# Optimization experiments

Measured on AMD Instinct MI355X. Metric: run time of the kernel, lower is better.

Reference implementation:

```python
import jax, jax.numpy as jnp
import numpy as np

B, N, E_PER_G = 32, 2048, 16384
NF, NHID, NCLS = 128, 128, 10
RATIO = 0.5
NT = B * N
E = B * E_PER_G
K1 = int(np.ceil(RATIO * N))        # 1024 nodes kept per graph after pool1
K2 = int(np.ceil(RATIO * K1))       # 512
K3 = int(np.ceil(RATIO * K2))       # 256


def setup_inputs() -> dict:
    key = jax.random.key(0)
    ks = jax.random.split(key, 16)
    x = jax.random.normal(ks[0], (NT, NF), dtype=jnp.float32)
    off = (jnp.arange(B, dtype=jnp.int32) * N)[:, None]
    src = (jax.random.randint(ks[1], (B, E_PER_G), 0, N, dtype=jnp.int32) + off).reshape(-1)
    dst = (jax.random.randint(ks[2], (B, E_PER_G), 0, N, dtype=jnp.int32) + off).reshape(-1)
    edge_index = jnp.stack([src, dst])
    batch = jnp.repeat(jnp.arange(B, dtype=jnp.int32), N)
    def lin(k, i, o):
        return jax.random.normal(k, (i, o), jnp.float32) / np.float32(np.sqrt(i))
    return {
        'x': x, 'edge_index': edge_index, 'batch': batch,
        'W1': lin(ks[3], NF, NHID), 'b1': jnp.zeros((NHID,), jnp.float32),
        'Wp1': lin(ks[4], NHID, 1), 'bp1': jnp.zeros((1,), jnp.float32),
        'W2': lin(ks[5], NHID, NHID), 'b2': jnp.zeros((NHID,), jnp.float32),
        'Wp2': lin(ks[6], NHID, 1), 'bp2': jnp.zeros((1,), jnp.float32),
        'W3': lin(ks[7], NHID, NHID), 'b3': jnp.zeros((NHID,), jnp.float32),
        'Wp3': lin(ks[8], NHID, 1), 'bp3': jnp.zeros((1,), jnp.float32),
        'lin1_W': lin(ks[9], 2 * NHID, NHID), 'lin1_b': jnp.zeros((NHID,), jnp.float32),
        'lin2_W': lin(ks[10], NHID, NHID // 2), 'lin2_b': jnp.zeros((NHID // 2,), jnp.float32),
        'lin3_W': lin(ks[11], NHID // 2, NCLS), 'lin3_b': jnp.zeros((NCLS,), jnp.float32),
    }


def gcn(x, src, dst, emask, nmask, W, b):
    # PyG GCNConv: add self-loops, symmetric normalization D^-1/2 (A+I) D^-1/2 @ (x W) + b.
    # Removed nodes/edges carry weight 0 via masks (equivalent to filter_adj re-indexing).
    h = x @ W
    deg = jnp.zeros((NT,), h.dtype).at[dst].add(emask) + nmask
    dinv = jnp.where(deg > 0, 1.0, 0.0) * jax.lax.rsqrt(jnp.where(deg > 0, deg, 1.0))
    coef = dinv[src] * dinv[dst] * emask               # [E]
    out = jnp.zeros_like(h).at[dst].add(coef[:, None] * h[src])
    out = out + ((dinv * dinv) * nmask)[:, None] * h   # self-loop term, norm = 1/deg
    return out + b


def sagpool(x, src, dst, emask, nmask, Wp, bp, k):
    # score = GCNConv(nhid,1); keep top-k per graph; x <- x[perm] * tanh(score[perm])
    score = gcn(x, src, dst, emask, nmask, Wp, bp)[:, 0]          # [NT]
    s = jnp.where(nmask > 0, score, -jnp.inf).reshape(B, N)
    _, idx = jax.lax.top_k(s, k)                                   # [B, k]
    keep = jnp.zeros((B, N), x.dtype).at[jnp.arange(B)[:, None], idx].set(1.0).reshape(-1)
    x_new = x * jnp.tanh(score)[:, None] * keep[:, None]
    emask_new = emask * keep[src] * keep[dst]                      # filter_adj
    return x_new, emask_new, keep


def readout(x, nmask, count):
    # [global_max_pool, global_mean_pool] over active nodes of each graph
    xb = x.reshape(B, N, -1)
    m = nmask.reshape(B, N, 1)
    mx = jnp.max(jnp.where(m > 0, xb, -jnp.inf), axis=1)
    mn = jnp.sum(xb * m, axis=1) / count
    return jnp.concatenate([mx, mn], axis=-1)


def reference(x, edge_index, batch, W1, b1, Wp1, bp1, W2, b2, Wp2, bp2,
              W3, b3, Wp3, bp3, lin1_W, lin1_b, lin2_W, lin2_b, lin3_W, lin3_b):
    src, dst = edge_index[0], edge_index[1]
    emask = jnp.ones((E,), x.dtype)
    nmask = jnp.ones((NT,), x.dtype)

    h = jax.nn.relu(gcn(x, src, dst, emask, nmask, W1, b1))
    h, emask, nmask = sagpool(h, src, dst, emask, nmask, Wp1, bp1, K1)
    x1 = readout(h, nmask, jnp.asarray(K1, x.dtype))

    h = jax.nn.relu(gcn(h, src, dst, emask, nmask, W2, b2))
    h, emask, nmask = sagpool(h, src, dst, emask, nmask, Wp2, bp2, K2)
    x2 = readout(h, nmask, jnp.asarray(K2, x.dtype))

    h = jax.nn.relu(gcn(h, src, dst, emask, nmask, W3, b3))
    h, emask, nmask = sagpool(h, src, dst, emask, nmask, Wp3, bp3, K3)
    x3 = readout(h, nmask, jnp.asarray(K3, x.dtype))

    g = x1 + x2 + x3
    g = jax.nn.relu(g @ lin1_W + lin1_b)   # dropout = identity in eval
    g = jax.nn.relu(g @ lin2_W + lin2_b)
    return jax.nn.log_softmax(g @ lin3_W + lin3_b, axis=-1)
```

## Files before the change

kernel.cpp:

```cpp
#include <hip/hip_runtime.h>
#include <math.h>


namespace {

constexpr int B_  = 32;
constexpr int N_  = 2048;
constexpr int NT  = B_ * N_;
constexpr int E_  = B_ * 16384;
constexpr int NCLS = 10;
constexpr int AST = 132;

__device__ __forceinline__ int relabel(int bpgsh) {
  int x = blockIdx.x & 7, slot = blockIdx.x >> 3;
  int g = x + 8 * (slot >> bpgsh);
  return (g << bpgsh) + (slot & ((1 << bpgsh) - 1));
}

__global__ void k_count(const int* __restrict__ dst, int* __restrict__ cnt) {
  int e = relabel(6) * 256 + threadIdx.x;
  atomicAdd(&cnt[dst[e]], 1);
}

__global__ void k_scan1(const int* __restrict__ cnt, int* __restrict__ off,
                        int* __restrict__ bsum) {
  __shared__ int s[256];
  int t = threadIdx.x;
  int i = blockIdx.x * 256 + t;
  int v = cnt[i];
  s[t] = v;
  __syncthreads();
  for (int d = 1; d < 256; d <<= 1) {
    int add = (t >= d) ? s[t - d] : 0;
    __syncthreads();
    s[t] += add;
    __syncthreads();
  }
  off[i] = s[t] - v;
  if (t == 255) bsum[blockIdx.x] = s[255];
}

__global__ void k_scan3(int* __restrict__ off, const int* __restrict__ bsum,
                        const int* __restrict__ cnt, int* __restrict__ cursor,
                        float* __restrict__ dinv, float* __restrict__ ds,
                        float* __restrict__ sws) {
  __shared__ int sb[256];
  int t = threadIdx.x;
  sb[t] = bsum[t];
  __syncthreads();
  for (int d = 1; d < 256; d <<= 1) {
    int add = (t >= d) ? sb[t - d] : 0;
    __syncthreads();
    sb[t] += add;
    __syncthreads();
  }
  int prefix = (blockIdx.x == 0) ? 0 : sb[blockIdx.x - 1];
  int i = blockIdx.x * 256 + t;
  int v = off[i] + prefix;
  off[i] = v;
  cursor[i] = v;
  if (i == NT - 1) off[NT] = E_;
  float d = 1.f + (float)cnt[i];
  float di = 1.f / sqrtf(d);
  dinv[i] = di;
  ds[i] = di;
  sws[i] = di * di;
}

__global__ void k_fill_srcp(const int* __restrict__ src, const int* __restrict__ dst,
                            int* __restrict__ cursor, int* __restrict__ srcp) {
  int e = relabel(6) * 256 + threadIdx.x;
  int p = atomicAdd(&cursor[dst[e]], 1);
  srcp[p] = src[e];
}

__global__ __launch_bounds__(256) void k_matmul(const float* __restrict__ A,
                                                const float* __restrict__ W,
                                                float* __restrict__ C,
                                                const int* __restrict__ kept,
                                                int kshift, int bpgsh,
                                                const float* __restrict__ scaleArr,
                                                float* __restrict__ pmx,
                                                float* __restrict__ psm) {
  __shared__ float Ast[2][32 * AST];
  __shared__ float Ws[2][32 * 128];
  __shared__ int rowid[128];
  __shared__ float rsc[128];
  const int tid = threadIdx.x;
  const int tile = relabel(bpgsh);
  if (kept) {
    if (tid < 128) {
      int q = tile * 128 + tid;
      int g = q >> kshift;
      int row = kept[g * N_ + (q - (g << kshift))];
      rowid[tid] = row;
      rsc[tid] = scaleArr[row];
    }
    __syncthreads();
  }
  const int rowq = tid >> 4;
  const int colq = tid & 15;
  float4 va[4], vw[4];
#pragma unroll
  for (int i = 0; i < 4; ++i) {
    int idx = tid + 256 * i;
    int row = idx & 127, fq = idx >> 7;
    int gr = kept ? rowid[row] : tile * 128 + row;
    va[i] = *(const float4*)&A[(size_t)gr * 128 + 4 * fq];
  }
#pragma unroll
  for (int i = 0; i < 4; ++i) {
    int idx = tid + 256 * i;
    int kk = idx >> 5, cf = idx & 31;
    vw[i] = *(const float4*)&W[(size_t)kk * 128 + 4 * cf];
  }
#pragma unroll
  for (int i = 0; i < 4; ++i) {
    int idx = tid + 256 * i;
    int row = idx & 127, fq = idx >> 7;
    Ast[0][(4 * fq + 0) * AST + row] = va[i].x;
    Ast[0][(4 * fq + 1) * AST + row] = va[i].y;
    Ast[0][(4 * fq + 2) * AST + row] = va[i].z;
    Ast[0][(4 * fq + 3) * AST + row] = va[i].w;
  }
#pragma unroll
  for (int i = 0; i < 4; ++i) {
    int idx = tid + 256 * i;
    int kk = idx >> 5, cf = idx & 31;
    *(float4*)&Ws[0][kk * 128 + 4 * cf] = vw[i];
  }
  __syncthreads();
  float acc[8][8] = {};
  for (int c = 0; c < 4; ++c) {
    int cur = c & 1;
    if (c < 3) {
      int k0n = 32 * (c + 1);
#pragma unroll
      for (int i = 0; i < 4; ++i) {
        int idx = tid + 256 * i;
        int row = idx & 127, fq = idx >> 7;
        int gr = kept ? rowid[row] : tile * 128 + row;
        va[i] = *(const float4*)&A[(size_t)gr * 128 + k0n + 4 * fq];
      }
#pragma unroll
      for (int i = 0; i < 4; ++i) {
        int idx = tid + 256 * i;
        int kk = idx >> 5, cf = idx & 31;
        vw[i] = *(const float4*)&W[(size_t)(k0n + kk) * 128 + 4 * cf];
      }
    }
#pragma unroll 2
    for (int kk = 0; kk < 32; ++kk) {
      float4 a0 = *(const float4*)&Ast[cur][kk * AST + 8 * rowq];
      float4 a1 = *(const float4*)&Ast[cur][kk * AST + 8 * rowq + 4];
      float4 w0 = *(const float4*)&Ws[cur][kk * 128 + 4 * colq];
      float4 w1 = *(const float4*)&Ws[cur][kk * 128 + 64 + 4 * colq];
      float a[8] = {a0.x, a0.y, a0.z, a0.w, a1.x, a1.y, a1.z, a1.w};
      float w[8] = {w0.x, w0.y, w0.z, w0.w, w1.x, w1.y, w1.z, w1.w};
#pragma unroll
      for (int r = 0; r < 8; ++r)
#pragma unroll
        for (int cc = 0; cc < 8; ++cc) acc[r][cc] += a[r] * w[cc];
    }
    if (kept) {
      int kkf = tid >> 3;
      int r0 = (tid & 7) * 16;
      float mxv = -INFINITY, smv = 0.f;
#pragma unroll
      for (int rr = 0; rr < 16; rr += 4) {
        float4 av = *(const float4*)&Ast[cur][kkf * AST + r0 + rr];
        float4 s4 = *(const float4*)&rsc[r0 + rr];
        float v0 = av.x * s4.x, v1 = av.y * s4.y;
        float v2 = av.z * s4.z, v3 = av.w * s4.w;
        mxv = fmaxf(fmaxf(fmaxf(mxv, v0), fmaxf(v1, v2)), v3);
        smv += v0 + v1 + v2 + v3;
      }
#pragma unroll
      for (int o = 4; o >= 1; o >>= 1) {
        mxv = fmaxf(mxv, __shfl_down(mxv, o));
        smv += __shfl_down(smv, o);
      }
      if ((tid & 7) == 0) {
        pmx[(size_t)tile * 128 + 32 * c + kkf] = mxv;
        psm[(size_t)tile * 128 + 32 * c + kkf] = smv;
      }
    }
    if (c < 3) {
      int nxt = cur ^ 1;
#pragma unroll
      for (int i = 0; i < 4; ++i) {
        int idx = tid + 256 * i;
        int row = idx & 127, fq = idx >> 7;
        Ast[nxt][(4 * fq + 0) * AST + row] = va[i].x;
        Ast[nxt][(4 * fq + 1) * AST + row] = va[i].y;
        Ast[nxt][(4 * fq + 2) * AST + row] = va[i].z;
        Ast[nxt][(4 * fq + 3) * AST + row] = va[i].w;
      }
#pragma unroll
      for (int i = 0; i < 4; ++i) {
        int idx = tid + 256 * i;
        int kk = idx >> 5, cf = idx & 31;
        *(float4*)&Ws[nxt][kk * 128 + 4 * cf] = vw[i];
      }
      __syncthreads();
    }
  }
#pragma unroll
  for (int r = 0; r < 8; ++r) {
    int gr = kept ? rowid[8 * rowq + r] : tile * 128 + 8 * rowq + r;
    float* Crow = &C[(size_t)gr * 128];
    *(float4*)&Crow[4 * colq] = make_float4(acc[r][0], acc[r][1], acc[r][2], acc[r][3]);
    *(float4*)&Crow[64 + 4 * colq] = make_float4(acc[r][4], acc[r][5], acc[r][6], acc[r][7]);
  }
}

__global__ __launch_bounds__(256) void k_agg(const float4* __restrict__ t4,
                                             const int* __restrict__ off,
                                             const int* __restrict__ srcp,
                                             const float* __restrict__ dinv,
                                             const float* __restrict__ ds,
                                             const float* __restrict__ sws,
                                             const float* __restrict__ bias,
                                             const float* __restrict__ Wp,
                                             float4* __restrict__ h4,
                                             float* __restrict__ t1,
                                             const int* __restrict__ kept,
                                             int kshift, int bpgsh) {
  int q = relabel(bpgsh) * 8 + (threadIdx.x >> 5);
  int node;
  if (kept) {
    int g = q >> kshift;
    node = kept[g * N_ + (q - (g << kshift))];
  } else {
    node = q;
  }
  const int lane = threadIdx.x & 31;
  const float dvi = dinv[node];
  float sw = sws[node];
  float4 self = t4[(size_t)node * 32 + lane];
  float4 acc = make_float4(sw * self.x, sw * self.y, sw * self.z, sw * self.w);
  int s = off[node], en = off[node + 1];
  int j = s;
  for (; j + 8 <= en; j += 8) {
    int sv[8];
    float cv[8];
#pragma unroll
    for (int i = 0; i < 8; ++i) sv[i] = srcp[j + i];
#pragma unroll
    for (int i = 0; i < 8; ++i) cv[i] = ds[sv[i]] * dvi;
#pragma unroll
    for (int i = 0; i < 8; ++i) {
      if (cv[i] != 0.f) {
        float4 r = t4[(size_t)sv[i] * 32 + lane];
        acc.x += cv[i] * r.x; acc.y += cv[i] * r.y;
        acc.z += cv[i] * r.z; acc.w += cv[i] * r.w;
      }
    }
  }
  for (; j < en; ++j) {
    int s0 = srcp[j];
    float c0 = ds[s0] * dvi;
    if (c0 != 0.f) {
      float4 r0 = t4[(size_t)s0 * 32 + lane];
      acc.x += c0 * r0.x; acc.y += c0 * r0.y; acc.z += c0 * r0.z; acc.w += c0 * r0.w;
    }
  }
  float4 b4 = ((const float4*)bias)[lane];
  acc.x = fmaxf(acc.x + b4.x, 0.f);
  acc.y = fmaxf(acc.y + b4.y, 0.f);
  acc.z = fmaxf(acc.z + b4.z, 0.f);
  acc.w = fmaxf(acc.w + b4.w, 0.f);
  h4[(size_t)node * 32 + lane] = acc;
  float4 wp = ((const float4*)Wp)[lane];
  float part = acc.x * wp.x + acc.y * wp.y + acc.z * wp.z + acc.w * wp.w;
#pragma unroll
  for (int o = 16; o > 0; o >>= 1) part += __shfl_down(part, o, 32);
  if (lane == 0) t1[node] = part;
}

__global__ __launch_bounds__(1024) void k_pool(const float* __restrict__ t1,
                                               const int* __restrict__ off,
                                               const int* __restrict__ srcp,
                                               float* __restrict__ dinv,
                                               float* __restrict__ ds,
                                               float* __restrict__ sws,
                                               float* __restrict__ scale,
                                               const float* __restrict__ bp,
                                               int* __restrict__ kept,
                                               const float4* __restrict__ h4,
                                               float* __restrict__ gout,
                                               float invk, int k) {
  __shared__ float st1[2048];
  __shared__ float sdv[2048];
  __shared__ float skp[2048];
  __shared__ int skept[1024];
  __shared__ unsigned rephist[4096];
  __shared__ unsigned ebits[64];
  __shared__ int wsum[16];
  __shared__ unsigned bc_digit, bc_prev;
  const int g = (blockIdx.x & 7) + 8 * (blockIdx.x >> 3);
  const int t = threadIdx.x;
  const int base = g * N_;
  st1[t] = t1[base + t];
  st1[t + 1024] = t1[base + t + 1024];
  sdv[t] = dinv[base + t];
  sdv[t + 1024] = dinv[base + t + 1024];
  if (t < 64) ebits[t] = 0u;
#pragma unroll
  for (int i = 0; i < 4; ++i) rephist[t + 1024 * i] = 0u;
  __syncthreads();
  float raw[2];
  unsigned key[2];
  float bpv = bp[0];
#pragma unroll
  for (int q = 0; q < 2; ++q) {
    int n = t + q * 1024;
    float di = sdv[n];
    float a = 0.f;
    int s = off[base + n], en = off[base + n + 1];
    int j = s;
    for (; j + 8 <= en; j += 8) {
      int sv[8];
#pragma unroll
      for (int i = 0; i < 8; ++i) sv[i] = srcp[j + i] - base;
#pragma unroll
      for (int i = 0; i < 8; ++i) a += sdv[sv[i]] * st1[sv[i]];
    }
    for (; j < en; ++j) {
      int sl = srcp[j] - base;
      a += sdv[sl] * st1[sl];
    }
    raw[q] = di * di * st1[n] + di * a + bpv;
    unsigned u = __float_as_uint(raw[q]);
    u = (u & 0x80000000u) ? ~u : (u | 0x80000000u);
    u = ~u;
    if (di <= 0.f) u = 0xFFFFFFFFu;
    key[q] = u;
  }
  unsigned prefix = 0u, rem = (unsigned)k;
  const int wv = t >> 6;
  for (int shift = 24; shift >= 0; shift -= 8) {
    unsigned mask = (shift == 24) ? 0u : (0xFFFFFFFFu << (shift + 8));
#pragma unroll
    for (int q = 0; q < 2; ++q)
      if ((key[q] & mask) == prefix)
        atomicAdd(&rephist[(wv << 8) + ((key[q] >> shift) & 255u)], 1u);
    __syncthreads();
    unsigned binv = 0u, v = 0u;
    if (t < 256) {
#pragma unroll
      for (int w = 0; w < 16; ++w) binv += rephist[(w << 8) + t];
      v = binv;
#pragma unroll
      for (int o = 1; o < 64; o <<= 1) {
        unsigned nv = __shfl_up(v, o);
        if ((t & 63) >= o) v += nv;
      }
      if ((t & 63) == 63) wsum[t >> 6] = (int)v;
    }
    __syncthreads();
    if (t < 256) {
      unsigned pre = 0u;
      int w4 = t >> 6;
      for (int u = 0; u < w4; ++u) pre += (unsigned)wsum[u];
      unsigned inc = v + pre, exc = inc - binv;
      if (inc >= rem && exc < rem) { bc_digit = (unsigned)t; bc_prev = exc; }
    }
    __syncthreads();
    if (shift > 0) {
#pragma unroll
      for (int i = 0; i < 4; ++i) rephist[t + 1024 * i] = 0u;
    }
    __syncthreads();
    prefix |= bc_digit << shift;
    rem -= bc_prev;
  }
  const unsigned Tkey = prefix;
  const int need = (int)rem;
#pragma unroll
  for (int q = 0; q < 2; ++q) {
    int n = t + q * 1024;
    if (key[q] == Tkey) atomicOr(&ebits[n >> 5], 1u << (n & 31));
  }
  __syncthreads();
#pragma unroll
  for (int q = 0; q < 2; ++q) {
    int n = t + q * 1024;
    float kp;
    if (key[q] < Tkey) {
      kp = 1.f;
    } else if (key[q] == Tkey) {
      int w = n >> 5;
      int rank = __popc(ebits[w] & ((1u << (n & 31)) - 1u));
      for (int u = 0; u < w; ++u) rank += __popc(ebits[u]);
      kp = (rank < need) ? 1.f : 0.f;
    } else {
      kp = 0.f;
    }
    skp[n] = kp;
    float sc = kp * tanhf(raw[q]);
    st1[n] = sc;
    scale[base + n] = sc;
  }
  __syncthreads();
  {
    int lane = t & 63, w = t >> 6;
    int a0 = (int)skp[2 * t], a1 = (int)skp[2 * t + 1];
    int ps = a0 + a1;
    int v = ps;
#pragma unroll
    for (int o = 1; o < 64; o <<= 1) {
      int nv = __shfl_up(v, o);
      if (lane >= o) v += nv;
    }
    if (lane == 63) wsum[w] = v;
    __syncthreads();
    if (t == 0) {
      int accv = 0;
      for (int i = 0; i < 16; ++i) { int tmp = wsum[i]; wsum[i] = accv; accv += tmp; }
    }
    __syncthreads();
    int excl = wsum[w] + v - ps;
    if (a0) { kept[base + excl] = base + 2 * t; skept[excl] = base + 2 * t; }
    if (a1) { kept[base + excl + a0] = base + 2 * t + 1; skept[excl + a0] = base + 2 * t + 1; }
  }
#pragma unroll
  for (int q = 0; q < 2; ++q) {
    int n = t + q * 1024;
    float nm = skp[n];
    float d = nm;
    int s = off[base + n], en = off[base + n + 1];
    int j = s;
    for (; j + 8 <= en; j += 8) {
      int sv[8];
#pragma unroll
      for (int i = 0; i < 8; ++i) sv[i] = srcp[j + i] - base;
#pragma unroll
      for (int i = 0; i < 8; ++i) d += skp[sv[i]];
    }
    for (; j < en; ++j) d += skp[srcp[j] - base];
    float di = (nm > 0.f) ? (1.f / sqrtf(d)) : 0.f;
    float sc = st1[n];
    dinv[base + n] = di;
    ds[base + n] = di * sc;
    sws[base + n] = di * di * sc;
  }
  if (!gout) return;
  __syncthreads();
  const int lane = t & 31, ng = t >> 5;
  float4 mx = make_float4(-INFINITY, -INFINITY, -INFINITY, -INFINITY);
  float4 sm = make_float4(0.f, 0.f, 0.f, 0.f);
  for (int i = ng; i < k; i += 32) {
    int node = skept[i];
    float sc = st1[node - base];
    float4 v = h4[(size_t)node * 32 + lane];
    v.x *= sc; v.y *= sc; v.z *= sc; v.w *= sc;
    mx.x = fmaxf(mx.x, v.x); mx.y = fmaxf(mx.y, v.y);
    mx.z = fmaxf(mx.z, v.z); mx.w = fmaxf(mx.w, v.w);
    sm.x += v.x; sm.y += v.y; sm.z += v.z; sm.w += v.w;
  }
  float4* red = (float4*)rephist;
  for (int d = 16; d >= 1; d >>= 1) {
    if (ng >= d && ng < 2 * d) {
      red[(ng - d) * 32 + lane] = mx;
      red[512 + (ng - d) * 32 + lane] = sm;
    }
    __syncthreads();
    if (ng < d) {
      float4 omx = red[ng * 32 + lane];
      float4 osm = red[512 + ng * 32 + lane];
      mx.x = fmaxf(mx.x, omx.x); mx.y = fmaxf(mx.y, omx.y);
      mx.z = fmaxf(mx.z, omx.z); mx.w = fmaxf(mx.w, omx.w);
      sm.x += osm.x; sm.y += osm.y; sm.z += osm.z; sm.w += osm.w;
    }
    __syncthreads();
  }
  if (ng == 0) {
    gout[g * 256 + 4 * lane + 0] = mx.x;
    gout[g * 256 + 4 * lane + 1] = mx.y;
    gout[g * 256 + 4 * lane + 2] = mx.z;
    gout[g * 256 + 4 * lane + 3] = mx.w;
    gout[g * 256 + 128 + 4 * lane + 0] = sm.x * invk;
    gout[g * 256 + 128 + 4 * lane + 1] = sm.y * invk;
    gout[g * 256 + 128 + 4 * lane + 2] = sm.z * invk;
    gout[g * 256 + 128 + 4 * lane + 3] = sm.w * invk;
  }
}

__global__ __launch_bounds__(128) void k_mlp(const float* __restrict__ pmxA,
                                             const float* __restrict__ psmA,
                                             const float* __restrict__ pmxB,
                                             const float* __restrict__ psmB,
                                             const float* __restrict__ goutC,
                                             const float* __restrict__ W1,
                                             const float* __restrict__ b1,
                                             const float* __restrict__ W2,
                                             const float* __restrict__ b2,
                                             const float* __restrict__ W3,
                                             const float* __restrict__ b3,
                                             float* __restrict__ out) {
  __shared__ float gr[256], o1[128], o2[64], o3[NCLS];
  int g = blockIdx.x, t = threadIdx.x;
  float mxA = -INFINITY, smA = 0.f;
#pragma unroll
  for (int p = 0; p < 8; ++p) {
    mxA = fmaxf(mxA, pmxA[(size_t)(g * 8 + p) * 128 + t]);
    smA += psmA[(size_t)(g * 8 + p) * 128 + t];
  }
  float mxB = -INFINITY, smB = 0.f;
#pragma unroll
  for (int p = 0; p < 4; ++p) {
    mxB = fmaxf(mxB, pmxB[(size_t)(g * 4 + p) * 128 + t]);
    smB += psmB[(size_t)(g * 4 + p) * 128 + t];
  }
  gr[t] = mxA + mxB + goutC[g * 256 + t];
  gr[t + 128] = smA * (1.f / 1024.f) + smB * (1.f / 512.f) + goutC[g * 256 + 128 + t];
  __syncthreads();
  float a = b1[t];
  for (int kk = 0; kk < 256; ++kk) a += gr[kk] * W1[kk * 128 + t];
  o1[t] = fmaxf(a, 0.f);
  __syncthreads();
  if (t < 64) {
    float a2 = b2[t];
    for (int kk = 0; kk < 128; ++kk) a2 += o1[kk] * W2[kk * 64 + t];
    o2[t] = fmaxf(a2, 0.f);
  }
  __syncthreads();
  if (t < NCLS) {
    float a3 = b3[t];
    for (int kk = 0; kk < 64; ++kk) a3 += o2[kk] * W3[kk * NCLS + t];
    o3[t] = a3;
  }
  __syncthreads();
  if (t == 0) {
    float m = -INFINITY;
    for (int c = 0; c < NCLS; ++c) m = fmaxf(m, o3[c]);
    float sum = 0.f;
    for (int c = 0; c < NCLS; ++c) sum += expf(o3[c] - m);
    float lse = logf(sum);
    for (int c = 0; c < NCLS; ++c) out[g * NCLS + c] = o3[c] - m - lse;
  }
}

}

extern "C" void kernel_launch(void* const* d_in, const int* in_sizes, int n_in,
                              void* d_out, int out_size, void* d_ws, size_t ws_size,
                              hipStream_t stream) {
  const float* x = (const float*)d_in[0];
  const int* ei = (const int*)d_in[1];
  const int* src = ei;
  const int* dst = ei + E_;
  const float* Wl[3]  = {(const float*)d_in[3], (const float*)d_in[7], (const float*)d_in[11]};
  const float* bl[3]  = {(const float*)d_in[4], (const float*)d_in[8], (const float*)d_in[12]};
  const float* Wpl[3] = {(const float*)d_in[5], (const float*)d_in[9], (const float*)d_in[13]};
  const float* bpl[3] = {(const float*)d_in[6], (const float*)d_in[10], (const float*)d_in[14]};
  const float* l1W = (const float*)d_in[15];
  const float* l1b = (const float*)d_in[16];
  const float* l2W = (const float*)d_in[17];
  const float* l2b = (const float*)d_in[18];
  const float* l3W = (const float*)d_in[19];
  const float* l3b = (const float*)d_in[20];

  char* p = (char*)d_ws;
  auto alloc = [&](size_t bytes) -> void* {
    void* r = (void*)p;
    p += (bytes + 255) & ~size_t(255);
    return r;
  };
  float* h      = (float*)alloc((size_t)NT * 128 * 4);
  float* t      = (float*)alloc((size_t)NT * 128 * 4);
  float* dinv   = (float*)alloc(NT * 4);
  float* ds     = (float*)alloc(NT * 4);
  float* sws    = (float*)alloc(NT * 4);
  float* scale  = (float*)alloc(NT * 4);
  float* t1     = (float*)alloc(NT * 4);
  int*   srcp   = (int*)alloc(E_ * 4);
  int*   off    = (int*)alloc((NT + 1) * 4);
  int*   cnt    = (int*)alloc(NT * 4);
  int*   cursor = (int*)alloc(NT * 4);
  int*   bsum   = (int*)alloc(256 * 4);
  int*   kept0  = (int*)alloc(NT * 4);
  int*   kept1  = (int*)alloc(NT * 4);
  int*   kept2  = (int*)alloc(NT * 4);
  float* pmxA   = (float*)alloc(256 * 128 * 4);
  float* psmA   = (float*)alloc(256 * 128 * 4);
  float* pmxB   = (float*)alloc(128 * 128 * 4);
  float* psmB   = (float*)alloc(128 * 128 * 4);
  float* goutC  = (float*)alloc(B_ * 256 * 4);

  int* keptL[3] = {kept0, kept1, kept2};
  const int K[3] = {1024, 512, 256};
  const int KSH[3] = {10, 9, 8};
  float* pmxL[3] = {nullptr, pmxA, pmxB};
  float* psmL[3] = {nullptr, psmA, psmB};

  hipMemsetAsync(cnt, 0, NT * 4, stream);

  k_count<<<E_ / 256, 256, 0, stream>>>(dst, cnt);
  k_scan1<<<256, 256, 0, stream>>>(cnt, off, bsum);
  k_scan3<<<256, 256, 0, stream>>>(off, bsum, cnt, cursor, dinv, ds, sws);
  k_fill_srcp<<<E_ / 256, 256, 0, stream>>>(src, dst, cursor, srcp);

  const float* inF = x;
  for (int l = 0; l < 3; ++l) {
    const int* inKept = (l == 0) ? nullptr : keptL[l - 1];
    int inKsh = (l == 0) ? 11 : KSH[l - 1];
    int nrows = (l == 0) ? NT : B_ * K[l - 1];
    int mm_bpgsh = (l == 0) ? 4 : (l == 1 ? 3 : 2);
    int ag_bpgsh = (l == 0) ? 8 : (l == 1 ? 7 : 6);
    k_matmul<<<nrows / 128, 256, 0, stream>>>(inF, Wl[l], t, inKept, inKsh, mm_bpgsh,
                                              scale, pmxL[l], psmL[l]);
    k_agg<<<nrows / 8, 256, 0, stream>>>((const float4*)t, off, srcp, dinv, ds, sws,
                                         bl[l], Wpl[l], (float4*)h, t1, inKept, inKsh,
                                         ag_bpgsh);
    k_pool<<<B_, 1024, 0, stream>>>(t1, off, srcp, dinv, ds, sws, scale, bpl[l],
                                    keptL[l], (const float4*)h,
                                    (l == 2) ? goutC : nullptr,
                                    1.f / (float)K[l], K[l]);
    inF = h;
  }
  k_mlp<<<B_, 128, 0, stream>>>(pmxA, psmA, pmxB, psmB, goutC,
                                l1W, l1b, l2W, l2b, l3W, l3b, (float*)d_out);
}
```

Baseline: 348.5 us.

## Halve matmul K-chunk to cut LDS and use 64-lane float2 aggregation

The matmul K-chunk drops from 32 to 16, which halves shared memory per block and doubles the number of pipeline stages. This should raise occupancy at the cost of more barriers. The aggregation kernel now gives each node a full 64-lane wavefront loading float2 instead of a 32-lane half-wave loading float4. That doubles the grid and the per-node thread count, so more gather requests are in flight, but the dot-product reduction gets longer. The block-to-graph relabel shifts are adjusted to match.

```diff
diff --git a/kernel.cpp b/kernel.cpp
--- a/kernel.cpp
+++ b/kernel.cpp
@@ -82,8 +82,8 @@
                                                 const float* __restrict__ scaleArr,
                                                 float* __restrict__ pmx,
                                                 float* __restrict__ psm) {
-  __shared__ float Ast[2][32 * AST];
-  __shared__ float Ws[2][32 * 128];
+  __shared__ float Ast[2][16 * AST];
+  __shared__ float Ws[2][16 * 128];
   __shared__ int rowid[128];
   __shared__ float rsc[128];
   const int tid = threadIdx.x;
@@ -100,57 +100,39 @@
   }
   const int rowq = tid >> 4;
   const int colq = tid & 15;
-  float4 va[4], vw[4];
-#pragma unroll
-  for (int i = 0; i < 4; ++i) {
-    int idx = tid + 256 * i;
-    int row = idx & 127, fq = idx >> 7;
-    int gr = kept ? rowid[row] : tile * 128 + row;
-    va[i] = *(const float4*)&A[(size_t)gr * 128 + 4 * fq];
-  }
-#pragma unroll
-  for (int i = 0; i < 4; ++i) {
-    int idx = tid + 256 * i;
-    int kk = idx >> 5, cf = idx & 31;
-    vw[i] = *(const float4*)&W[(size_t)kk * 128 + 4 * cf];
-  }
-#pragma unroll
-  for (int i = 0; i < 4; ++i) {
-    int idx = tid + 256 * i;
-    int row = idx & 127, fq = idx >> 7;
-    Ast[0][(4 * fq + 0) * AST + row] = va[i].x;
-    Ast[0][(4 * fq + 1) * AST + row] = va[i].y;
-    Ast[0][(4 * fq + 2) * AST + row] = va[i].z;
-    Ast[0][(4 * fq + 3) * AST + row] = va[i].w;
-  }
-#pragma unroll
-  for (int i = 0; i < 4; ++i) {
-    int idx = tid + 256 * i;
-    int kk = idx >> 5, cf = idx & 31;
-    *(float4*)&Ws[0][kk * 128 + 4 * cf] = vw[i];
+  const int arow = tid & 127, afq = tid >> 7;
+  const int wkk = tid >> 5, wcf = tid & 31;
+  float4 va[2], vw[2];
+#pragma unroll
+  for (int i = 0; i < 2; ++i) {
+    int gr = kept ? rowid[arow] : tile * 128 + arow;
+    va[i] = *(const float4*)&A[(size_t)gr * 128 + 4 * (afq + 2 * i)];
+    vw[i] = *(const float4*)&W[(size_t)(wkk + 8 * i) * 128 + 4 * wcf];
+  }
+#pragma unroll
+  for (int i = 0; i < 2; ++i) {
+    int fq = afq + 2 * i;
+    Ast[0][(4 * fq + 0) * AST + arow] = va[i].x;
+    Ast[0][(4 * fq + 1) * AST + arow] = va[i].y;
+    Ast[0][(4 * fq + 2) * AST + arow] = va[i].z;
+    Ast[0][(4 * fq + 3) * AST + arow] = va[i].w;
+    *(float4*)&Ws[0][(wkk + 8 * i) * 128 + 4 * wcf] = vw[i];
   }
   __syncthreads();
   float acc[8][8] = {};
-  for (int c = 0; c < 4; ++c) {
+  for (int c = 0; c < 8; ++c) {
     int cur = c & 1;
-    if (c < 3) {
-      int k0n = 32 * (c + 1);
-#pragma unroll
-      for (int i = 0; i < 4; ++i) {
-        int idx = tid + 256 * i;
-        int row = idx & 127, fq = idx >> 7;
-        int gr = kept ? rowid[row] : tile * 128 + row;
-        va[i] = *(const float4*)&A[(size_t)gr * 128 + k0n + 4 * fq];
+    if (c < 7) {
+      int k0n = 16 * (c + 1);
+      int gr = kept ? rowid[arow] : tile * 128 + arow;
+#pragma unroll
+      for (int i = 0; i < 2; ++i) {
+        va[i] = *(const float4*)&A[(size_t)gr * 128 + k0n + 4 * (afq + 2 * i)];
+        vw[i] = *(const float4*)&W[(size_t)(k0n + wkk + 8 * i) * 128 + 4 * wcf];
       }
-#pragma unroll
-      for (int i = 0; i < 4; ++i) {
-        int idx = tid + 256 * i;
-        int kk = idx >> 5, cf = idx & 31;
-        vw[i] = *(const float4*)&W[(size_t)(k0n + kk) * 128 + 4 * cf];
-      }
-    }
-#pragma unroll 2
-    for (int kk = 0; kk < 32; ++kk) {
+    }
+#pragma unroll
+    for (int kk = 0; kk < 16; ++kk) {
       float4 a0 = *(const float4*)&Ast[cur][kk * AST + 8 * rowq];
       float4 a1 = *(const float4*)&Ast[cur][kk * AST + 8 * rowq + 4];
       float4 w0 = *(const float4*)&Ws[cur][kk * 128 + 4 * colq];
@@ -163,11 +145,11 @@
         for (int cc = 0; cc < 8; ++cc) acc[r][cc] += a[r] * w[cc];
     }
     if (kept) {
-      int kkf = tid >> 3;
-      int r0 = (tid & 7) * 16;
+      int kkf = tid >> 4;
+      int r0 = (tid & 15) * 8;
       float mxv = -INFINITY, smv = 0.f;
 #pragma unroll
-      for (int rr = 0; rr < 16; rr += 4) {
+      for (int rr = 0; rr < 8; rr += 4) {
         float4 av = *(const float4*)&Ast[cur][kkf * AST + r0 + rr];
         float4 s4 = *(const float4*)&rsc[r0 + rr];
         float v0 = av.x * s4.x, v1 = av.y * s4.y;
@@ -176,31 +158,25 @@
         smv += v0 + v1 + v2 + v3;
       }
 #pragma unroll
-      for (int o = 4; o >= 1; o >>= 1) {
+      for (int o = 8; o >= 1; o >>= 1) {
         mxv = fmaxf(mxv, __shfl_down(mxv, o));
         smv += __shfl_down(smv, o);
       }
-      if ((tid & 7) == 0) {
-        pmx[(size_t)tile * 128 + 32 * c + kkf] = mxv;
-        psm[(size_t)tile * 128 + 32 * c + kkf] = smv;
+      if ((tid & 15) == 0) {
+        pmx[(size_t)tile * 128 + 16 * c + kkf] = mxv;
+        psm[(size_t)tile * 128 + 16 * c + kkf] = smv;
       }
     }
-    if (c < 3) {
+    if (c < 7) {
       int nxt = cur ^ 1;
 #pragma unroll
-      for (int i = 0; i < 4; ++i) {
-        int idx = tid + 256 * i;
-        int row = idx & 127, fq = idx >> 7;
-        Ast[nxt][(4 * fq + 0) * AST + row] = va[i].x;
-        Ast[nxt][(4 * fq + 1) * AST + row] = va[i].y;
-        Ast[nxt][(4 * fq + 2) * AST + row] = va[i].z;
-        Ast[nxt][(4 * fq + 3) * AST + row] = va[i].w;
-      }
-#pragma unroll
-      for (int i = 0; i < 4; ++i) {
-        int idx = tid + 256 * i;
-        int kk = idx >> 5, cf = idx & 31;
-        *(float4*)&Ws[nxt][kk * 128 + 4 * cf] = vw[i];
+      for (int i = 0; i < 2; ++i) {
+        int fq = afq + 2 * i;
+        Ast[nxt][(4 * fq + 0) * AST + arow] = va[i].x;
+        Ast[nxt][(4 * fq + 1) * AST + arow] = va[i].y;
+        Ast[nxt][(4 * fq + 2) * AST + arow] = va[i].z;
+        Ast[nxt][(4 * fq + 3) * AST + arow] = va[i].w;
+        *(float4*)&Ws[nxt][(wkk + 8 * i) * 128 + 4 * wcf] = vw[i];
       }
       __syncthreads();
     }
@@ -214,7 +190,7 @@
   }
 }
 
-__global__ __launch_bounds__(256) void k_agg(const float4* __restrict__ t4,
+__global__ __launch_bounds__(256) void k_agg(const float2* __restrict__ t2,
                                              const int* __restrict__ off,
                                              const int* __restrict__ srcp,
                                              const float* __restrict__ dinv,
@@ -222,11 +198,11 @@
                                              const float* __restrict__ sws,
                                              const float* __restrict__ bias,
                                              const float* __restrict__ Wp,
-                                             float4* __restrict__ h4,
+                                             float2* __restrict__ h2,
                                              float* __restrict__ t1,
                                              const int* __restrict__ kept,
                                              int kshift, int bpgsh) {
-  int q = relabel(bpgsh) * 8 + (threadIdx.x >> 5);
+  int q = relabel(bpgsh) * 4 + (threadIdx.x >> 6);
   int node;
   if (kept) {
     int g = q >> kshift;
@@ -234,11 +210,11 @@
   } else {
     node = q;
   }
-  const int lane = threadIdx.x & 31;
+  const int lane = threadIdx.x & 63;
   const float dvi = dinv[node];
   float sw = sws[node];
-  float4 self = t4[(size_t)node * 32 + lane];
-  float4 acc = make_float4(sw * self.x, sw * self.y, sw * self.z, sw * self.w);
+  float2 self = t2[(size_t)node * 64 + lane];
+  float2 acc = make_float2(sw * self.x, sw * self.y);
   int s = off[node], en = off[node + 1];
   int j = s;
   for (; j + 8 <= en; j += 8) {
@@ -251,9 +227,9 @@
 #pragma unroll
     for (int i = 0; i < 8; ++i) {
       if (cv[i] != 0.f) {
-        float4 r = t4[(size_t)sv[i] * 32 + lane];
-        acc.x += cv[i] * r.x; acc.y += cv[i] * r.y;
-        acc.z += cv[i] * r.z; acc.w += cv[i] * r.w;
+        float2 r = t2[(size_t)sv[i] * 64 + lane];
+        acc.x += cv[i] * r.x;
+        acc.y += cv[i] * r.y;
       }
     }
   }
@@ -261,20 +237,19 @@
     int s0 = srcp[j];
     float c0 = ds[s0] * dvi;
     if (c0 != 0.f) {
-      float4 r0 = t4[(size_t)s0 * 32 + lane];
-      acc.x += c0 * r0.x; acc.y += c0 * r0.y; acc.z += c0 * r0.z; acc.w += c0 * r0.w;
-    }
-  }
-  float4 b4 = ((const float4*)bias)[lane];
-  acc.x = fmaxf(acc.x + b4.x, 0.f);
-  acc.y = fmaxf(acc.y + b4.y, 0.f);
-  acc.z = fmaxf(acc.z + b4.z, 0.f);
-  acc.w = fmaxf(acc.w + b4.w, 0.f);
-  h4[(size_t)node * 32 + lane] = acc;
-  float4 wp = ((const float4*)Wp)[lane];
-  float part = acc.x * wp.x + acc.y * wp.y + acc.z * wp.z + acc.w * wp.w;
-#pragma unroll
-  for (int o = 16; o > 0; o >>= 1) part += __shfl_down(part, o, 32);
+      float2 r0 = t2[(size_t)s0 * 64 + lane];
+      acc.x += c0 * r0.x;
+      acc.y += c0 * r0.y;
+    }
+  }
+  float2 b2 = ((const float2*)bias)[lane];
+  acc.x = fmaxf(acc.x + b2.x, 0.f);
+  acc.y = fmaxf(acc.y + b2.y, 0.f);
+  h2[(size_t)node * 64 + lane] = acc;
+  float2 wp = ((const float2*)Wp)[lane];
+  float part = acc.x * wp.x + acc.y * wp.y;
+#pragma unroll
+  for (int o = 32; o > 0; o >>= 1) part += __shfl_down(part, o);
   if (lane == 0) t1[node] = part;
 }
 
@@ -608,11 +583,11 @@
     int inKsh = (l == 0) ? 11 : KSH[l - 1];
     int nrows = (l == 0) ? NT : B_ * K[l - 1];
     int mm_bpgsh = (l == 0) ? 4 : (l == 1 ? 3 : 2);
-    int ag_bpgsh = (l == 0) ? 8 : (l == 1 ? 7 : 6);
+    int ag_bpgsh = (l == 0) ? 9 : (l == 1 ? 8 : 7);
     k_matmul<<<nrows / 128, 256, 0, stream>>>(inF, Wl[l], t, inKept, inKsh, mm_bpgsh,
                                               scale, pmxL[l], psmL[l]);
-    k_agg<<<nrows / 8, 256, 0, stream>>>((const float4*)t, off, srcp, dinv, ds, sws,
-                                         bl[l], Wpl[l], (float4*)h, t1, inKept, inKsh,
+    k_agg<<<nrows / 4, 256, 0, stream>>>((const float2*)t, off, srcp, dinv, ds, sws,
+                                         bl[l], Wpl[l], (float2*)h, t1, inKept, inKsh,
                                          ag_bpgsh);
     k_pool<<<B_, 1024, 0, stream>>>(t1, off, srcp, dinv, ds, sws, scale, bpl[l],
                                     keptL[l], (const float4*)h,
```

After: 405.4 us. 1.16x slower.

## Fuse CSR construction into one per-graph kernel with shared-memory histogram

Applied to the files above, without the earlier changes.

Replaces the memset plus four kernels (global atomic count, two-level scan, atomic fill) with a single kernel that uses one block per graph. Each block builds a degree histogram in shared memory, scans it with wave shuffles, writes offsets and degree normalizers, then scatters source indices using shared-memory atomic cursors. This removes launch overhead, global atomics and intermediate buffers. The cost is that only 32 blocks run, so GPU occupancy during CSR build is low, and it relies on edges being grouped per graph.

```diff
diff --git a/kernel.cpp b/kernel.cpp
--- a/kernel.cpp
+++ b/kernel.cpp
@@ -7,7 +7,8 @@
 constexpr int B_  = 32;
 constexpr int N_  = 2048;
 constexpr int NT  = B_ * N_;
-constexpr int E_  = B_ * 16384;
+constexpr int EPG = 16384;
+constexpr int E_  = B_ * EPG;
 constexpr int NCLS = 10;
 constexpr int AST = 132;
 
@@ -17,61 +18,69 @@
   return (g << bpgsh) + (slot & ((1 << bpgsh) - 1));
 }
 
-__global__ void k_count(const int* __restrict__ dst, int* __restrict__ cnt) {
-  int e = relabel(6) * 256 + threadIdx.x;
-  atomicAdd(&cnt[dst[e]], 1);
-}
-
-__global__ void k_scan1(const int* __restrict__ cnt, int* __restrict__ off,
-                        int* __restrict__ bsum) {
-  __shared__ int s[256];
-  int t = threadIdx.x;
-  int i = blockIdx.x * 256 + t;
-  int v = cnt[i];
-  s[t] = v;
-  __syncthreads();
-  for (int d = 1; d < 256; d <<= 1) {
-    int add = (t >= d) ? s[t - d] : 0;
-    __syncthreads();
-    s[t] += add;
-    __syncthreads();
-  }
-  off[i] = s[t] - v;
-  if (t == 255) bsum[blockIdx.x] = s[255];
-}
-
-__global__ void k_scan3(int* __restrict__ off, const int* __restrict__ bsum,
-                        const int* __restrict__ cnt, int* __restrict__ cursor,
-                        float* __restrict__ dinv, float* __restrict__ ds,
-                        float* __restrict__ sws) {
-  __shared__ int sb[256];
-  int t = threadIdx.x;
-  sb[t] = bsum[t];
-  __syncthreads();
-  for (int d = 1; d < 256; d <<= 1) {
-    int add = (t >= d) ? sb[t - d] : 0;
-    __syncthreads();
-    sb[t] += add;
-    __syncthreads();
-  }
-  int prefix = (blockIdx.x == 0) ? 0 : sb[blockIdx.x - 1];
-  int i = blockIdx.x * 256 + t;
-  int v = off[i] + prefix;
-  off[i] = v;
-  cursor[i] = v;
-  if (i == NT - 1) off[NT] = E_;
-  float d = 1.f + (float)cnt[i];
-  float di = 1.f / sqrtf(d);
-  dinv[i] = di;
-  ds[i] = di;
-  sws[i] = di * di;
-}
-
-__global__ void k_fill_srcp(const int* __restrict__ src, const int* __restrict__ dst,
-                            int* __restrict__ cursor, int* __restrict__ srcp) {
-  int e = relabel(6) * 256 + threadIdx.x;
-  int p = atomicAdd(&cursor[dst[e]], 1);
-  srcp[p] = src[e];
+__global__ __launch_bounds__(1024) void k_csr(const int* __restrict__ src,
+                                              const int* __restrict__ dst,
+                                              int* __restrict__ off,
+                                              int* __restrict__ srcp,
+                                              float* __restrict__ dinv,
+                                              float* __restrict__ ds,
+                                              float* __restrict__ sws) {
+  __shared__ int hist[2048];
+  __shared__ int wsum[16];
+  const int g = blockIdx.x;
+  const int t = threadIdx.x;
+  const int base_n = g * N_;
+  const int base_e = g * EPG;
+  hist[t] = 0;
+  hist[t + 1024] = 0;
+  __syncthreads();
+#pragma unroll
+  for (int i = 0; i < EPG / 1024; ++i) {
+    int d = dst[base_e + t + 1024 * i];
+    atomicAdd(&hist[d - base_n], 1);
+  }
+  __syncthreads();
+  int a0 = hist[2 * t], a1 = hist[2 * t + 1];
+  int ps = a0 + a1;
+  {
+    int lane = t & 63, w = t >> 6;
+    int v = ps;
+#pragma unroll
+    for (int o = 1; o < 64; o <<= 1) {
+      int nv = __shfl_up(v, o);
+      if (lane >= o) v += nv;
+    }
+    if (lane == 63) wsum[w] = v;
+    __syncthreads();
+    if (t == 0) {
+      int accv = 0;
+      for (int i = 0; i < 16; ++i) { int tmp = wsum[i]; wsum[i] = accv; accv += tmp; }
+    }
+    __syncthreads();
+    int excl = wsum[w] + v - ps;
+    off[base_n + 2 * t] = base_e + excl;
+    off[base_n + 2 * t + 1] = base_e + excl + a0;
+    hist[2 * t] = excl;
+    hist[2 * t + 1] = excl + a0;
+    float d0 = 1.f + (float)a0, d1 = 1.f + (float)a1;
+    float di0 = 1.f / sqrtf(d0), di1 = 1.f / sqrtf(d1);
+    dinv[base_n + 2 * t] = di0;
+    dinv[base_n + 2 * t + 1] = di1;
+    ds[base_n + 2 * t] = di0;
+    ds[base_n + 2 * t + 1] = di1;
+    sws[base_n + 2 * t] = di0 * di0;
+    sws[base_n + 2 * t + 1] = di1 * di1;
+    if (g == B_ - 1 && t == 0) off[NT] = E_;
+  }
+  __syncthreads();
+#pragma unroll
+  for (int i = 0; i < EPG / 1024; ++i) {
+    int e = base_e + t + 1024 * i;
+    int d = dst[e];
+    int s = src[e];
+    int slot = atomicAdd(&hist[d - base_n], 1);
+    srcp[base_e + slot] = s;
+  }
 }
 
 __global__ __launch_bounds__(256) void k_matmul(const float* __restrict__ A,
@@ -577,9 +586,6 @@
   float* t1     = (float*)alloc(NT * 4);
   int*   srcp   = (int*)alloc(E_ * 4);
   int*   off    = (int*)alloc((NT + 1) * 4);
-  int*   cnt    = (int*)alloc(NT * 4);
-  int*   cursor = (int*)alloc(NT * 4);
-  int*   bsum   = (int*)alloc(256 * 4);
   int*   kept0  = (int*)alloc(NT * 4);
   int*   kept1  = (int*)alloc(NT * 4);
   int*   kept2  = (int*)alloc(NT * 4);
@@ -595,12 +601,7 @@
   float* pmxL[3] = {nullptr, pmxA, pmxB};
   float* psmL[3] = {nullptr, psmA, psmB};
 
-  hipMemsetAsync(cnt, 0, NT * 4, stream);
-
-  k_count<<<E_ / 256, 256, 0, stream>>>(dst, cnt);
-  k_scan1<<<256, 256, 0, stream>>>(cnt, off, bsum);
-  k_scan3<<<256, 256, 0, stream>>>(off, bsum, cnt, cursor, dinv, ds, sws);
-  k_fill_srcp<<<E_ / 256, 256, 0, stream>>>(src, dst, cursor, srcp);
+  k_csr<<<B_, 1024, 0, stream>>>(src, dst, off, srcp, dinv, ds, sws);
 
   const float* inF = x;
   for (int l = 0; l < 3; ++l) {
```

Measured after the change: 324.3 us. 1.07x faster.
